# Performance work log

Hardware: AMD Instinct MI355X
Metric: run time of the kernel (lower is better)

The kernel has to match this reference:

```python
import jax, jax.numpy as jnp
import numpy as np

B, L, U, H = 16, 1024, 512, 2  # batch, seq_len, units, highway_num


def setup_inputs() -> dict:
    key = jax.random.key(0)
    ks = jax.random.split(key, 8)
    s = 0.02  # weight init scale
    return {
        "inputs": jax.random.normal(ks[0], (B, L, U), dtype=jnp.float32),
        "tW": jax.random.normal(ks[1], (H, U, U), dtype=jnp.float32) * s,
        "tb": jnp.zeros((H, U), dtype=jnp.float32),
        "cW": jax.random.normal(ks[2], (H, U, U), dtype=jnp.float32) * s,
        "cb": jnp.zeros((H, U), dtype=jnp.float32),
        "aW": jax.random.normal(ks[3], (3 * U,), dtype=jnp.float32) * s,
        "ab": jnp.zeros((1,), dtype=jnp.float32),
        "frW": jax.random.normal(ks[4], (2 * U, U), dtype=jnp.float32) * s,
        "frb": jnp.zeros((U,), dtype=jnp.float32),
        "ffW": jax.random.normal(ks[5], (2 * U, U), dtype=jnp.float32) * s,
        "ffb": jnp.zeros((U,), dtype=jnp.float32),
    }


def reference(inputs, tW, tb, cW, cb, aW, ab, frW, frb, ffW, ffb):
    # Highway stack (inference: dropout is identity)
    x = inputs
    for i in range(tW.shape[0]):
        t = jax.nn.relu(x @ tW[i] + tb[i])
        c = jax.nn.sigmoid(x @ cW[i] + cb[i])
        x = t * c + x * (1.0 - c)

    # Pairwise MLP self-attention.
    # Original: A_ij = relu(dense1(concat([x_i, x_j, x_i*x_j]))).
    # Split aW = [w1; w2; w3] so we never materialize the [B,L,L,3U] tensor:
    # A_ij = relu(x_i.w1 + x_j.w2 + sum_d x_i_d * x_j_d * w3_d + b)
    u = x.shape[-1]
    w1, w2, w3 = aW[:u], aW[u:2 * u], aW[2 * u:]
    s1 = x @ w1                                    # [B,L]
    s2 = x @ w2                                    # [B,L]
    s3 = jnp.einsum('bid,bjd->bij', x * w3, x)     # [B,L,L]
    A = jax.nn.relu(s1[:, :, None] + s2[:, None, :] + s3 + ab[0])
    att = jnp.einsum('bij,bjd->bid', jax.nn.softmax(A, axis=-1), x)

    # Fuse gate. NOTE: original code uses fuse_f_dense (sigmoid) for BOTH
    # z and f (fuse_z_dense is never called), so z == f at inference.
    concat = jnp.concatenate([inputs, att], axis=-1)  # [B,L,2U]
    z = jax.nn.sigmoid(concat @ ffW + ffb)
    r = jax.nn.sigmoid(concat @ frW + frb)
    f = z
    return r * inputs + f * z
```

## Files before the change

kernel.cpp:

```cpp
#include <hip/hip_runtime.h>
#include <math.h>

typedef __bf16 bf16;
typedef __attribute__((ext_vector_type(8))) __bf16 bf16x8;
typedef __attribute__((ext_vector_type(4))) float f32x4;

#define CDIV(a,b) (((a)+(b)-1)/(b))


__device__ __forceinline__ void load_lds16(const bf16* g, bf16* l) {
  __builtin_amdgcn_global_load_lds(
      (const __attribute__((address_space(1))) unsigned int*)(g),
      (__attribute__((address_space(3))) unsigned int*)(l), 16, 0, 0);
}

struct GemmArgs {
  const bf16* A; const bf16* B; bf16* C;
  int K, lda, ldb, ldc;
  long long Ab, Bb, Cb;
  const float* s1; const float* s2; const float* abp;
  float* lsum;
  int L;
  int gxsh, gysh;
};

template<int EPI, int TN>
__global__ __launch_bounds__(256, 4)
void gemm_nt(GemmArgs g) {
  constexpr int JN = TN / 32;
  __shared__ bf16 As[128 * 64];
  __shared__ bf16 Bs[TN * 64];
  const int tid = threadIdx.x;
  const int bid = blockIdx.x;
  const int xcd = bid & 7;
  const int t = bid >> 3;
  const int bx = t & ((1 << g.gxsh) - 1);
  const int r  = t >> g.gxsh;
  const int Rx = gridDim.x >> (3 + g.gxsh);
  const int gr = xcd * Rx + r;
  const int by = gr & ((1 << g.gysh) - 1);
  const int bz = gr >> g.gysh;

  const bf16* Ag = g.A + (long long)bz * g.Ab + (long long)(by * 128) * g.lda;
  const bf16* Bg = g.B + (long long)bz * g.Bb + (long long)(bx * TN) * g.ldb;
  const int wid = tid >> 6, lane = tid & 63;
  const int wm = (wid >> 1) << 6;
  const int wn = (wid & 1) * (TN / 2);
  const int lr = lane & 15, lq = lane >> 4;

  f32x4 acc[4][JN];
#pragma unroll
  for (int i = 0; i < 4; i++)
#pragma unroll
    for (int j = 0; j < JN; j++) acc[i][j] = f32x4{0.f, 0.f, 0.f, 0.f};

  const int srow8 = (tid >> 3) & 7;
  const int skc   = (tid & 7) ^ srow8;
  const int lswz  = (lr & 7);

  for (int k0 = 0; k0 < g.K; k0 += 64) {
    __syncthreads();
#pragma unroll
    for (int j = 0; j < 4; j++) {
      const int ci = (tid >> 6) * 4 + j;
      const int row = ci * 8 + srow8;
      load_lds16(Ag + (long long)row * g.lda + k0 + skc * 8, As + ci * 512);
    }
#pragma unroll
    for (int j = 0; j < JN; j++) {
      const int ci = (tid >> 6) * JN + j;
      const int row = ci * 8 + srow8;
      load_lds16(Bg + (long long)row * g.ldb + k0 + skc * 8, Bs + ci * 512);
    }
    __syncthreads();
#pragma unroll
    for (int ks = 0; ks < 2; ks++) {
      bf16x8 af[4], bfr[JN];
      const int kx = (ks * 4 + lq) ^ lswz;
#pragma unroll
      for (int i = 0; i < 4; i++)
        af[i] = *(const bf16x8*)(&As[(wm + i * 16 + lr) * 64 + kx * 8]);
#pragma unroll
      for (int j = 0; j < JN; j++)
        bfr[j] = *(const bf16x8*)(&Bs[(wn + j * 16 + lr) * 64 + kx * 8]);
#pragma unroll
      for (int i = 0; i < 4; i++)
#pragma unroll
        for (int j = 0; j < JN; j++)
          acc[i][j] = __builtin_amdgcn_mfma_f32_16x16x32_bf16(af[i], bfr[j], acc[i][j], 0, 0, 0);
    }
  }

  bf16* Cg = g.C + (long long)bz * g.Cb;
#pragma unroll
  for (int i = 0; i < 4; i++) {
#pragma unroll
    for (int v = 0; v < 4; v++) {
      int row = by * 128 + wm + i * 16 + lq * 4 + v;
      float srow = 0.f;
      if (EPI == 1) srow = g.s1[bz * g.L + row] + g.abp[0];
      if (EPI == 4) srow = 1.f / g.s1[bz * g.L + row];
      float psum = 0.f;
#pragma unroll
      for (int j = 0; j < JN; j++) {
        int col = bx * TN + wn + j * 16 + lr;
        float val = acc[i][j][v];
        if (EPI == 1) {
          val += srow + g.s2[bz * g.L + col];
          val = fminf(fmaxf(val, 0.f), 60.f);
          val = __expf(val);
          bf16 eb = (bf16)val;
          psum += (float)eb;
          Cg[(long long)row * g.ldc + col] = eb;
        } else {
          val *= srow;
          Cg[(long long)row * g.ldc + col] = (bf16)val;
        }
      }
      if (EPI == 1) {
        psum += __shfl_xor(psum, 1, 64);
        psum += __shfl_xor(psum, 2, 64);
        psum += __shfl_xor(psum, 4, 64);
        psum += __shfl_xor(psum, 8, 64);
        if (lr == 0) atomicAdd(&g.lsum[bz * g.L + row], psum);
      }
    }
  }
}

struct DualArgs {
  const bf16* A; const bf16* A2;
  const bf16* Bt;
  void* C; const void* xres;
  const float* bias_t; const float* bias_c;
  int K, ldb;
  const float* aW;
  float* s1a; float* s2a;
  bf16* q;
  bf16* xT;
};

template<int EPI>
__global__ __launch_bounds__(256, 4)
void gemm_dual(DualArgs g) {
  __shared__ bf16 smem[2 * 128 * 64];
  bf16* As = smem;
  bf16* Bs = smem + 8192;
  const int tid = threadIdx.x;
  const int bid = blockIdx.x;
  const int xcd = bid & 7;
  const int t = bid >> 3;
  const int bx = t & 7;
  const int r  = t >> 3;
  const int Rx = gridDim.x >> 6;
  const int by = xcd * Rx + r;

  const int wid = tid >> 6, lane = tid & 63;
  const int wm = (wid >> 1) << 6;
  const int wn = (wid & 1) << 6;
  const int lr = lane & 15, lq = lane >> 4;

  f32x4 acc[4][4];
#pragma unroll
  for (int i = 0; i < 4; i++)
#pragma unroll
    for (int j = 0; j < 4; j++) acc[i][j] = f32x4{0.f, 0.f, 0.f, 0.f};

  const int srow8 = (tid >> 3) & 7;
  const int skc   = (tid & 7) ^ srow8;
  const int lswz  = (lr & 7);
  const long long abase = (long long)(by * 128) * 512;

  for (int k0 = 0; k0 < g.K; k0 += 64) {
    const bf16* Ak = (k0 < 512) ? g.A : g.A2;
    const int kk = k0 & 511;
    __syncthreads();
#pragma unroll
    for (int j = 0; j < 4; j++) {
      const int ci = (tid >> 6) * 4 + j;
      const int bn = ci * 8 + srow8;
      load_lds16(Ak + abase + (long long)bn * 512 + kk + skc * 8, As + ci * 512);
      const int grp = bn >> 5, r5 = bn & 31;
      const int grow = ((grp & 1) << 9) + bx * 64 + ((grp >> 1) << 5) + r5;
      load_lds16(g.Bt + (long long)grow * g.ldb + k0 + skc * 8, Bs + ci * 512);
    }
    __syncthreads();
#pragma unroll
    for (int ks = 0; ks < 2; ks++) {
      bf16x8 af[4], bfr[4];
      const int kx = (ks * 4 + lq) ^ lswz;
#pragma unroll
      for (int i = 0; i < 4; i++)
        af[i] = *(const bf16x8*)(&As[(wm + i * 16 + lr) * 64 + kx * 8]);
#pragma unroll
      for (int j = 0; j < 4; j++)
        bfr[j] = *(const bf16x8*)(&Bs[(wn + j * 16 + lr) * 64 + kx * 8]);
#pragma unroll
      for (int i = 0; i < 4; i++)
#pragma unroll
        for (int j = 0; j < 4; j++)
          acc[i][j] = __builtin_amdgcn_mfma_f32_16x16x32_bf16(af[i], bfr[j], acc[i][j], 0, 0, 0);
    }
  }

  const int colb = bx * 64 + (wn >> 1);
  bf16 xn_arr[4][4][2];
#pragma unroll
  for (int i = 0; i < 4; i++) {
#pragma unroll
    for (int v = 0; v < 4; v++) {
      int row = by * 128 + wm + i * 16 + lq * 4 + v;
      float p1s = 0.f, p2s = 0.f;
#pragma unroll
      for (int j = 0; j < 2; j++) {
        int col = colb + j * 16 + lr;
        long long idx = (long long)row * 512 + col;
        float p0 = acc[i][j][v] + g.bias_t[col];
        float p1 = acc[i][j + 2][v] + g.bias_c[col];
        if (EPI == 1) {
          float z = 1.f / (1.f + __expf(-p0));
          float rr = 1.f / (1.f + __expf(-p1));
          float x = (float)((const bf16*)g.xres)[idx];
          ((float*)g.C)[idx] = rr * x + z * z;
        } else {
          float tt = fmaxf(p0, 0.f);
          float c = 1.f / (1.f + __expf(-p1));
          float x = (float)((const bf16*)g.xres)[idx];
          bf16 xn = (bf16)(tt * c + x * (1.f - c));
          ((bf16*)g.C)[idx] = xn;
          if (EPI == 2) {
            xn_arr[i][v][j] = xn;
            float xf = (float)xn;
            p1s += xf * g.aW[col];
            p2s += xf * g.aW[512 + col];
            g.q[idx] = (bf16)(xf * g.aW[1024 + col]);
          }
        }
      }
      if (EPI == 2) {
        p1s += __shfl_xor(p1s, 1, 64);
        p1s += __shfl_xor(p1s, 2, 64);
        p1s += __shfl_xor(p1s, 4, 64);
        p1s += __shfl_xor(p1s, 8, 64);
        p2s += __shfl_xor(p2s, 1, 64);
        p2s += __shfl_xor(p2s, 2, 64);
        p2s += __shfl_xor(p2s, 4, 64);
        p2s += __shfl_xor(p2s, 8, 64);
        if (lr == 0) {
          atomicAdd(&g.s1a[row], p1s);
          atomicAdd(&g.s2a[row], p2s);
        }
      }
    }
  }

  if (EPI == 2) {
    bf16* Ts = smem;
    __syncthreads();
#pragma unroll
    for (int i = 0; i < 4; i++)
#pragma unroll
      for (int v = 0; v < 4; v++)
#pragma unroll
        for (int j = 0; j < 2; j++) {
          int rloc = wm + i * 16 + lq * 4 + v;
          int cloc = (wn >> 1) + j * 16 + lr;
          Ts[cloc * 136 + rloc] = xn_arr[i][v][j];
        }
    __syncthreads();
    const int b = by >> 3;
    bf16* dst = g.xT + (long long)b * 524288 + ((by & 7) * 128);
#pragma unroll
    for (int it = 0; it < 2; it++) {
      int d = (tid >> 3) + it * 32;
      int jb = (tid & 7) * 16;
      bf16x8 v0 = *(const bf16x8*)(&Ts[d * 136 + jb]);
      bf16x8 v1 = *(const bf16x8*)(&Ts[d * 136 + jb + 8]);
      long long o = (long long)(bx * 64 + d) * 1024 + jb;
      *(bf16x8*)(dst + o) = v0;
      *(bf16x8*)(dst + o + 8) = v1;
    }
  }
}

__device__ __forceinline__ void tile_transpose(const float* src, int sld,
                                               bf16* dst, int dld,
                                               int k0, int n0, int tid) {
  __shared__ float tile[64][65];
  const int rr = tid >> 4, c4 = (tid & 15) * 4;
#pragma unroll
  for (int it = 0; it < 4; it++) {
    int r = rr + it * 16;
    f32x4 v = *(const f32x4*)(src + (long long)(k0 + r) * sld + n0 + c4);
    tile[r][c4] = v[0]; tile[r][c4 + 1] = v[1];
    tile[r][c4 + 2] = v[2]; tile[r][c4 + 3] = v[3];
  }
  __syncthreads();
  const int nl = tid >> 2, kb = (tid & 3) * 16;
  bf16x8 o0, o1;
#pragma unroll
  for (int kk = 0; kk < 8; kk++) o0[kk] = (bf16)tile[kb + kk][nl];
#pragma unroll
  for (int kk = 0; kk < 8; kk++) o1[kk] = (bf16)tile[kb + 8 + kk][nl];
  bf16* d = dst + (long long)(n0 + nl) * dld + k0 + kb;
  *(bf16x8*)d = o0;
  *(bf16x8*)(d + 8) = o1;
}

__global__ void prep(const float* tW, const float* tb, const float* cW, const float* cb,
                     const float* frW, const float* frb, const float* ffW, const float* ffb,
                     const float* inp, bf16* xb0,
                     bf16* w1T, bf16* w2T, float* bias1, float* bias2, float* sred) {
  const int bid = blockIdx.x, tid = threadIdx.x;
  if (bid < 256) {
    const int quad = bid >> 6, tile = bid & 63;
    const int l = quad >> 1, half = quad & 1;
    const float* src = (half ? cW : tW) + l * 262144;
    bf16* dst = w1T + l * 524288 + half * 262144;
    tile_transpose(src, 512, dst, 512, (tile >> 3) * 64, (tile & 7) * 64, tid);
  } else if (bid < 512) {
    const int j = bid - 256;
    const int half = j >> 7, tile = j & 127;
    const float* src = half ? frW : ffW;
    bf16* dst = w2T + half * 524288;
    tile_transpose(src, 512, dst, 1024, (tile >> 3) * 64, (tile & 7) * 64, tid);
  } else if (bid < 4608) {
    long long i8 = (((long long)(bid - 512)) * 256 + tid) * 8;
    bf16x8 o;
#pragma unroll
    for (int k = 0; k < 8; k++) o[k] = (bf16)inp[i8 + k];
    *(bf16x8*)(xb0 + i8) = o;
  } else {
    for (int j = tid; j < 3072; j += 256) {
      if (j < 2048) {
        int l = j >> 10, n = j & 1023;
        bias1[j] = (n < 512) ? tb[l * 512 + n] : cb[l * 512 + (n - 512)];
      } else {
        int n = j - 2048;
        bias2[n] = (n < 512) ? ffb[n] : frb[n - 512];
      }
    }
    for (int j = tid; j < 12288; j += 256)
      *(f32x4*)(sred + j * 4) = f32x4{0.f, 0.f, 0.f, 0.f};
  }
}

extern "C" void kernel_launch(void* const* d_in, const int* in_sizes, int n_in,
                              void* d_out, int out_size, void* d_ws, size_t ws_size,
                              hipStream_t stream) {
  const float* inp = (const float*)d_in[0];
  const float* tW  = (const float*)d_in[1];
  const float* tb  = (const float*)d_in[2];
  const float* cW  = (const float*)d_in[3];
  const float* cb  = (const float*)d_in[4];
  const float* aW  = (const float*)d_in[5];
  const float* ab  = (const float*)d_in[6];
  const float* frW = (const float*)d_in[7];
  const float* frb = (const float*)d_in[8];
  const float* ffW = (const float*)d_in[9];
  const float* ffb = (const float*)d_in[10];
  float* out = (float*)d_out;

  char* p = (char*)d_ws;
  auto alloc = [&](size_t bytes) { char* r = p; p += (bytes + 255) & ~size_t(255); return r; };
  bf16* xb0   = (bf16*) alloc(16777216);
  bf16* x1    = (bf16*) alloc(16777216);
  bf16* x2    = (bf16*) alloc(16777216);
  bf16* q16   = (bf16*) alloc(16777216);
  bf16* xT16  = (bf16*) alloc(16777216);
  bf16* att16 = (bf16*) alloc(16777216);
  bf16* E16   = (bf16*) alloc(33554432);
  float* sred = (float*)alloc(196608);
  bf16* w1T   = (bf16*) alloc(2097152);
  bf16* w2T   = (bf16*) alloc(2097152);
  float* bias1= (float*)alloc(8192);
  float* bias2= (float*)alloc(4096);
  float* s1 = sred, *s2 = sred + 16384, *lsum = sred + 32768;

  prep<<<4609, 256, 0, stream>>>(
      tW, tb, cW, cb, frW, frb, ffW, ffb, inp, xb0, w1T, w2T, bias1, bias2, sred);

  {
    DualArgs g{};
    g.A = xb0; g.A2 = xb0; g.Bt = w1T;
    g.C = x1; g.xres = xb0;
    g.bias_t = bias1; g.bias_c = bias1 + 512;
    g.K = 512; g.ldb = 512;
    gemm_dual<0><<<1024, 256, 0, stream>>>(g);
  }
  {
    DualArgs g{};
    g.A = x1; g.A2 = x1; g.Bt = w1T + 524288;
    g.C = x2; g.xres = x1;
    g.bias_t = bias1 + 1024; g.bias_c = bias1 + 1536;
    g.K = 512; g.ldb = 512;
    g.aW = aW; g.s1a = s1; g.s2a = s2; g.q = q16; g.xT = xT16;
    gemm_dual<2><<<1024, 256, 0, stream>>>(g);
  }
  {
    GemmArgs g{};
    g.A = q16; g.B = x2; g.C = E16;
    g.K = 512; g.lda = 512; g.ldb = 512; g.ldc = 1024;
    g.Ab = 524288; g.Bb = 524288; g.Cb = 1048576;
    g.s1 = s1; g.s2 = s2; g.abp = ab; g.lsum = lsum; g.L = 1024;
    g.gxsh = 3; g.gysh = 3;
    gemm_nt<1, 128><<<1024, 256, 0, stream>>>(g);
  }
  {
    GemmArgs g{};
    g.A = E16; g.B = xT16; g.C = att16;
    g.K = 1024; g.lda = 1024; g.ldb = 1024; g.ldc = 512;
    g.Ab = 1048576; g.Bb = 524288; g.Cb = 524288;
    g.s1 = lsum; g.L = 1024;
    g.gxsh = 3; g.gysh = 3;
    gemm_nt<4, 64><<<1024, 256, 0, stream>>>(g);
  }
  {
    DualArgs g{};
    g.A = xb0; g.A2 = att16; g.Bt = w2T;
    g.C = out; g.xres = xb0;
    g.bias_t = bias2; g.bias_c = bias2 + 512;
    g.K = 1024; g.ldb = 1024;
    gemm_dual<1><<<1024, 256, 0, stream>>>(g);
  }
}
```

Measured before the change: 269.7 us.

## Rewrite dual highway GEMMs as 256x256 8-wave double-buffered pipelined kernel

The dual-output highway/fuse GEMM moves from 128x128 tiles with 4 waves and a single-buffered LDS loop to 256x256 tiles (128 output columns per gate) with 8 waves. Global-to-LDS loads are double-buffered and interleaved in quarter stages with MFMA phases, using s_setprio and explicit vmcnt waits. The xT transpose now writes straight into LDS during the epilogue. The aim is more data reuse per tile and overlap of loads with compute. The trade-offs are a grid of only 256 blocks, fewer blocks per CU from the larger LDS footprint, and fragile hand-written barrier and waitcnt ordering.

```diff
diff --git a/kernel.cpp b/kernel.cpp
--- a/kernel.cpp
+++ b/kernel.cpp
@@ -4,8 +4,6 @@
 typedef __bf16 bf16;
 typedef __attribute__((ext_vector_type(8))) __bf16 bf16x8;
 typedef __attribute__((ext_vector_type(4))) float f32x4;
-
-#define CDIV(a,b) (((a)+(b)-1)/(b))
 
 
 __device__ __forceinline__ void load_lds16(const bf16* g, bf16* l) {
@@ -141,82 +139,156 @@
 };
 
 template<int EPI>
-__global__ __launch_bounds__(256, 4)
-void gemm_dual(DualArgs g) {
-  __shared__ bf16 smem[2 * 128 * 64];
-  bf16* As = smem;
-  bf16* Bs = smem + 8192;
+__global__ __launch_bounds__(512, 2)
+void gemm_dual8(DualArgs g) {
+  __shared__ __align__(16) bf16 smem[2][32768];
   const int tid = threadIdx.x;
   const int bid = blockIdx.x;
   const int xcd = bid & 7;
   const int t = bid >> 3;
-  const int bx = t & 7;
-  const int r  = t >> 3;
-  const int Rx = gridDim.x >> 6;
-  const int by = xcd * Rx + r;
-
+  const int bx = t & 3;
+  const int by = xcd * 8 + (t >> 2);
   const int wid = tid >> 6, lane = tid & 63;
-  const int wm = (wid >> 1) << 6;
-  const int wn = (wid & 1) << 6;
+  const int wr = wid >> 2, wc = wid & 3;
   const int lr = lane & 15, lq = lane >> 4;
-
-  f32x4 acc[4][4];
-#pragma unroll
-  for (int i = 0; i < 4; i++)
+  const int lswz = lr & 7;
+  const int srow8 = (lane >> 3) & 7;
+  const int skc = (lane & 7) ^ srow8;
+  const long long abase = (long long)(by * 256) * 512;
+  const int NT = g.K >> 6;
+
+  f32x4 acc[8][4];
+#pragma unroll
+  for (int i = 0; i < 8; i++)
 #pragma unroll
     for (int j = 0; j < 4; j++) acc[i][j] = f32x4{0.f, 0.f, 0.f, 0.f};
 
-  const int srow8 = (tid >> 3) & 7;
-  const int skc   = (tid & 7) ^ srow8;
-  const int lswz  = (lr & 7);
-  const long long abase = (long long)(by * 128) * 512;
-
-  for (int k0 = 0; k0 < g.K; k0 += 64) {
-    const bf16* Ak = (k0 < 512) ? g.A : g.A2;
-    const int kk = k0 & 511;
-    __syncthreads();
-#pragma unroll
-    for (int j = 0; j < 4; j++) {
-      const int ci = (tid >> 6) * 4 + j;
-      const int bn = ci * 8 + srow8;
-      load_lds16(Ak + abase + (long long)bn * 512 + kk + skc * 8, As + ci * 512);
+  auto stage_a = [&](int kt, int b, int h) {
+    const bf16* Ak = (kt < 8) ? g.A : g.A2;
+    const int kk = (kt & 7) << 6;
+#pragma unroll
+    for (int jj = 0; jj < 2; jj++) {
+      const int c = h * 16 + wid * 2 + jj;
+      const int row = c * 8 + srow8;
+      load_lds16(Ak + abase + (long long)row * 512 + kk + skc * 8,
+                 &smem[b][c * 512]);
+    }
+  };
+  auto stage_b = [&](int kt, int b, int h) {
+    const int k0 = kt << 6;
+#pragma unroll
+    for (int jj = 0; jj < 2; jj++) {
+      const int ci = wid * 2 + jj;
+      const int c = ((ci >> 2) << 3) + (h << 2) + (ci & 3);
+      const int bn = c * 8 + srow8;
       const int grp = bn >> 5, r5 = bn & 31;
-      const int grow = ((grp & 1) << 9) + bx * 64 + ((grp >> 1) << 5) + r5;
-      load_lds16(g.Bt + (long long)grow * g.ldb + k0 + skc * 8, Bs + ci * 512);
-    }
-    __syncthreads();
-#pragma unroll
-    for (int ks = 0; ks < 2; ks++) {
-      bf16x8 af[4], bfr[4];
-      const int kx = (ks * 4 + lq) ^ lswz;
-#pragma unroll
-      for (int i = 0; i < 4; i++)
-        af[i] = *(const bf16x8*)(&As[(wm + i * 16 + lr) * 64 + kx * 8]);
-#pragma unroll
-      for (int j = 0; j < 4; j++)
-        bfr[j] = *(const bf16x8*)(&Bs[(wn + j * 16 + lr) * 64 + kx * 8]);
-#pragma unroll
-      for (int i = 0; i < 4; i++)
-#pragma unroll
-        for (int j = 0; j < 4; j++)
-          acc[i][j] = __builtin_amdgcn_mfma_f32_16x16x32_bf16(af[i], bfr[j], acc[i][j], 0, 0, 0);
-    }
-  }
-
-  const int colb = bx * 64 + (wn >> 1);
-  bf16 xn_arr[4][4][2];
-#pragma unroll
-  for (int i = 0; i < 4; i++) {
+      const int grow = ((grp & 1) << 9) + bx * 128 + ((grp >> 1) << 5) + r5;
+      load_lds16(g.Bt + (long long)grow * g.ldb + k0 + skc * 8,
+                 &smem[b][16384 + c * 512]);
+    }
+  };
+  auto ldA = [&](int b, int i, int ks) -> bf16x8 {
+    const int kx = (ks * 4 + lq) ^ lswz;
+    return *(const bf16x8*)(&smem[b][(wr * 128 + i * 16 + lr) * 64 + kx * 8]);
+  };
+  auto ldB = [&](int b, int j, int ks) -> bf16x8 {
+    const int kx = (ks * 4 + lq) ^ lswz;
+    return *(const bf16x8*)(&smem[b][16384 + (wc * 64 + j * 16 + lr) * 64 + kx * 8]);
+  };
+
+  stage_b(0, 0, 0); stage_b(0, 0, 1); stage_a(0, 0, 0); stage_a(0, 0, 1);
+  stage_b(1, 1, 0); stage_b(1, 1, 1); stage_a(1, 1, 0);
+  asm volatile("s_waitcnt vmcnt(6)" ::: "memory");
+  __builtin_amdgcn_s_barrier();
+
+  for (int kt = 0; kt < NT; kt++) {
+    const int cur = kt & 1, nxt = cur ^ 1;
+    bf16x8 af[4][2], b01[2][2], b23[2][2];
+    if (kt + 1 < NT) stage_a(kt + 1, nxt, 1);
+#pragma unroll
+    for (int i = 0; i < 4; i++)
+#pragma unroll
+      for (int ks = 0; ks < 2; ks++) af[i][ks] = ldA(cur, i, ks);
+#pragma unroll
+    for (int j = 0; j < 2; j++)
+#pragma unroll
+      for (int ks = 0; ks < 2; ks++) b01[j][ks] = ldB(cur, j, ks);
+    __builtin_amdgcn_s_barrier();
+    __builtin_amdgcn_s_setprio(1);
+#pragma unroll
+    for (int i = 0; i < 4; i++)
+#pragma unroll
+      for (int j = 0; j < 2; j++)
+#pragma unroll
+        for (int ks = 0; ks < 2; ks++)
+          acc[i][j] = __builtin_amdgcn_mfma_f32_16x16x32_bf16(af[i][ks], b01[j][ks], acc[i][j], 0, 0, 0);
+    __builtin_amdgcn_s_setprio(0);
+    __builtin_amdgcn_s_barrier();
+    if (kt + 2 < NT) stage_b(kt + 2, cur, 0);
+#pragma unroll
+    for (int j = 0; j < 2; j++)
+#pragma unroll
+      for (int ks = 0; ks < 2; ks++) b23[j][ks] = ldB(cur, 2 + j, ks);
+    __builtin_amdgcn_s_barrier();
+    __builtin_amdgcn_s_setprio(1);
+#pragma unroll
+    for (int i = 0; i < 4; i++)
+#pragma unroll
+      for (int j = 0; j < 2; j++)
+#pragma unroll
+        for (int ks = 0; ks < 2; ks++)
+          acc[i][2 + j] = __builtin_amdgcn_mfma_f32_16x16x32_bf16(af[i][ks], b23[j][ks], acc[i][2 + j], 0, 0, 0);
+    __builtin_amdgcn_s_setprio(0);
+    __builtin_amdgcn_s_barrier();
+    if (kt + 2 < NT) stage_b(kt + 2, cur, 1);
+#pragma unroll
+    for (int i = 0; i < 4; i++)
+#pragma unroll
+      for (int ks = 0; ks < 2; ks++) af[i][ks] = ldA(cur, 4 + i, ks);
+    __builtin_amdgcn_s_barrier();
+    __builtin_amdgcn_s_setprio(1);
+#pragma unroll
+    for (int i = 0; i < 4; i++)
+#pragma unroll
+      for (int j = 0; j < 2; j++)
+#pragma unroll
+        for (int ks = 0; ks < 2; ks++)
+          acc[4 + i][2 + j] = __builtin_amdgcn_mfma_f32_16x16x32_bf16(af[i][ks], b23[j][ks], acc[4 + i][2 + j], 0, 0, 0);
+    __builtin_amdgcn_s_setprio(0);
+    __builtin_amdgcn_s_barrier();
+    if (kt + 2 < NT) stage_a(kt + 2, cur, 0);
+    __builtin_amdgcn_s_barrier();
+    __builtin_amdgcn_s_setprio(1);
+#pragma unroll
+    for (int i = 0; i < 4; i++)
+#pragma unroll
+      for (int j = 0; j < 2; j++)
+#pragma unroll
+        for (int ks = 0; ks < 2; ks++)
+          acc[4 + i][j] = __builtin_amdgcn_mfma_f32_16x16x32_bf16(af[i][ks], b01[j][ks], acc[4 + i][j], 0, 0, 0);
+    __builtin_amdgcn_s_setprio(0);
+    if (kt + 2 < NT) {
+      asm volatile("s_waitcnt vmcnt(6)" ::: "memory");
+    } else if (kt + 1 < NT) {
+      asm volatile("s_waitcnt vmcnt(0)" ::: "memory");
+    }
+    __builtin_amdgcn_s_barrier();
+  }
+
+  bf16* Ts = (bf16*)&smem[0][0];
+  const int colb = bx * 128 + wc * 32;
+#pragma unroll
+  for (int i = 0; i < 8; i++) {
 #pragma unroll
     for (int v = 0; v < 4; v++) {
-      int row = by * 128 + wm + i * 16 + lq * 4 + v;
+      const int row = by * 256 + wr * 128 + i * 16 + lq * 4 + v;
       float p1s = 0.f, p2s = 0.f;
 #pragma unroll
-      for (int j = 0; j < 2; j++) {
-        int col = colb + j * 16 + lr;
-        long long idx = (long long)row * 512 + col;
-        float p0 = acc[i][j][v] + g.bias_t[col];
-        float p1 = acc[i][j + 2][v] + g.bias_c[col];
+      for (int jj = 0; jj < 2; jj++) {
+        const int col = colb + jj * 16 + lr;
+        const long long idx = (long long)row * 512 + col;
+        float p0 = acc[i][jj][v] + g.bias_t[col];
+        float p1 = acc[i][jj + 2][v] + g.bias_c[col];
         if (EPI == 1) {
           float z = 1.f / (1.f + __expf(-p0));
           float rr = 1.f / (1.f + __expf(-p1));
@@ -229,11 +301,11 @@
           bf16 xn = (bf16)(tt * c + x * (1.f - c));
           ((bf16*)g.C)[idx] = xn;
           if (EPI == 2) {
-            xn_arr[i][v][j] = xn;
             float xf = (float)xn;
             p1s += xf * g.aW[col];
             p2s += xf * g.aW[512 + col];
             g.q[idx] = (bf16)(xf * g.aW[1024 + col]);
+            Ts[(wc * 32 + jj * 16 + lr) * 264 + (wr * 128 + i * 16 + lq * 4 + v)] = xn;
           }
         }
       }
@@ -255,28 +327,18 @@
   }
 
   if (EPI == 2) {
-    bf16* Ts = smem;
     __syncthreads();
-#pragma unroll
-    for (int i = 0; i < 4; i++)
-#pragma unroll
-      for (int v = 0; v < 4; v++)
-#pragma unroll
-        for (int j = 0; j < 2; j++) {
-          int rloc = wm + i * 16 + lq * 4 + v;
-          int cloc = (wn >> 1) + j * 16 + lr;
-          Ts[cloc * 136 + rloc] = xn_arr[i][v][j];
-        }
-    __syncthreads();
-    const int b = by >> 3;
-    bf16* dst = g.xT + (long long)b * 524288 + ((by & 7) * 128);
-#pragma unroll
-    for (int it = 0; it < 2; it++) {
-      int d = (tid >> 3) + it * 32;
-      int jb = (tid & 7) * 16;
-      bf16x8 v0 = *(const bf16x8*)(&Ts[d * 136 + jb]);
-      bf16x8 v1 = *(const bf16x8*)(&Ts[d * 136 + jb + 8]);
-      long long o = (long long)(bx * 64 + d) * 1024 + jb;
+    const int b = by >> 2;
+    const long long j0 = (long long)(by & 3) * 256;
+    bf16* dst = g.xT + (long long)b * 524288;
+    const int dloc = tid >> 2;
+    const int jb = (tid & 3) * 64;
+#pragma unroll
+    for (int it = 0; it < 4; it++) {
+      const int j = jb + it * 16;
+      bf16x8 v0 = *(const bf16x8*)(&Ts[dloc * 264 + j]);
+      bf16x8 v1 = *(const bf16x8*)(&Ts[dloc * 264 + j + 8]);
+      long long o = (long long)(bx * 128 + dloc) * 1024 + j0 + j;
       *(bf16x8*)(dst + o) = v0;
       *(bf16x8*)(dst + o + 8) = v1;
     }
@@ -386,7 +448,7 @@
     g.C = x1; g.xres = xb0;
     g.bias_t = bias1; g.bias_c = bias1 + 512;
     g.K = 512; g.ldb = 512;
-    gemm_dual<0><<<1024, 256, 0, stream>>>(g);
+    gemm_dual8<0><<<256, 512, 0, stream>>>(g);
   }
   {
     DualArgs g{};
@@ -395,7 +457,7 @@
     g.bias_t = bias1 + 1024; g.bias_c = bias1 + 1536;
     g.K = 512; g.ldb = 512;
     g.aW = aW; g.s1a = s1; g.s2a = s2; g.q = q16; g.xT = xT16;
-    gemm_dual<2><<<1024, 256, 0, stream>>>(g);
+    gemm_dual8<2><<<256, 512, 0, stream>>>(g);
   }
   {
     GemmArgs g{};
@@ -421,6 +483,6 @@
     g.C = out; g.xres = xb0;
     g.bias_t = bias2; g.bias_c = bias2 + 512;
     g.K = 1024; g.ldb = 1024;
-    gemm_dual<1><<<1024, 256, 0, stream>>>(g);
-  }
-}
+    gemm_dual8<1><<<256, 512, 0, stream>>>(g);
+  }
+}
```

Measured after the change: 296.7 us. 1.1x slower.

## Fuse score GEMM, exp epilogue and PV GEMM into one attention kernel

Applied to the files above, without the earlier changes.

Replaces the two batched GEMM launches with a single fused attention kernel. The score GEMM, its exp epilogue and the value GEMM no longer write a full [B,L,L] bf16 score matrix to global memory and read it back. Each 512-thread block keeps a 64-row Q tile resident in LDS and streams X tiles through a double buffer. It writes exp scores into a swizzled LDS tile, multiplies them with X^T fetched straight from global memory, and normalises by row sums reduced in LDS instead of with global atomics. This trades the large intermediate traffic and one launch for a grid of only 256 blocks with heavy LDS use, low occupancy, frequent barriers, and uncached, partly redundant global loads of X^T.

```diff
diff --git a/kernel.cpp b/kernel.cpp
--- a/kernel.cpp
+++ b/kernel.cpp
@@ -4,128 +4,12 @@
 typedef __bf16 bf16;
 typedef __attribute__((ext_vector_type(8))) __bf16 bf16x8;
 typedef __attribute__((ext_vector_type(4))) float f32x4;
-
-#define CDIV(a,b) (((a)+(b)-1)/(b))
 
 
 __device__ __forceinline__ void load_lds16(const bf16* g, bf16* l) {
   __builtin_amdgcn_global_load_lds(
       (const __attribute__((address_space(1))) unsigned int*)(g),
       (__attribute__((address_space(3))) unsigned int*)(l), 16, 0, 0);
-}
-
-struct GemmArgs {
-  const bf16* A; const bf16* B; bf16* C;
-  int K, lda, ldb, ldc;
-  long long Ab, Bb, Cb;
-  const float* s1; const float* s2; const float* abp;
-  float* lsum;
-  int L;
-  int gxsh, gysh;
-};
-
-template<int EPI, int TN>
-__global__ __launch_bounds__(256, 4)
-void gemm_nt(GemmArgs g) {
-  constexpr int JN = TN / 32;
-  __shared__ bf16 As[128 * 64];
-  __shared__ bf16 Bs[TN * 64];
-  const int tid = threadIdx.x;
-  const int bid = blockIdx.x;
-  const int xcd = bid & 7;
-  const int t = bid >> 3;
-  const int bx = t & ((1 << g.gxsh) - 1);
-  const int r  = t >> g.gxsh;
-  const int Rx = gridDim.x >> (3 + g.gxsh);
-  const int gr = xcd * Rx + r;
-  const int by = gr & ((1 << g.gysh) - 1);
-  const int bz = gr >> g.gysh;
-
-  const bf16* Ag = g.A + (long long)bz * g.Ab + (long long)(by * 128) * g.lda;
-  const bf16* Bg = g.B + (long long)bz * g.Bb + (long long)(bx * TN) * g.ldb;
-  const int wid = tid >> 6, lane = tid & 63;
-  const int wm = (wid >> 1) << 6;
-  const int wn = (wid & 1) * (TN / 2);
-  const int lr = lane & 15, lq = lane >> 4;
-
-  f32x4 acc[4][JN];
-#pragma unroll
-  for (int i = 0; i < 4; i++)
-#pragma unroll
-    for (int j = 0; j < JN; j++) acc[i][j] = f32x4{0.f, 0.f, 0.f, 0.f};
-
-  const int srow8 = (tid >> 3) & 7;
-  const int skc   = (tid & 7) ^ srow8;
-  const int lswz  = (lr & 7);
-
-  for (int k0 = 0; k0 < g.K; k0 += 64) {
-    __syncthreads();
-#pragma unroll
-    for (int j = 0; j < 4; j++) {
-      const int ci = (tid >> 6) * 4 + j;
-      const int row = ci * 8 + srow8;
-      load_lds16(Ag + (long long)row * g.lda + k0 + skc * 8, As + ci * 512);
-    }
-#pragma unroll
-    for (int j = 0; j < JN; j++) {
-      const int ci = (tid >> 6) * JN + j;
-      const int row = ci * 8 + srow8;
-      load_lds16(Bg + (long long)row * g.ldb + k0 + skc * 8, Bs + ci * 512);
-    }
-    __syncthreads();
-#pragma unroll
-    for (int ks = 0; ks < 2; ks++) {
-      bf16x8 af[4], bfr[JN];
-      const int kx = (ks * 4 + lq) ^ lswz;
-#pragma unroll
-      for (int i = 0; i < 4; i++)
-        af[i] = *(const bf16x8*)(&As[(wm + i * 16 + lr) * 64 + kx * 8]);
-#pragma unroll
-      for (int j = 0; j < JN; j++)
-        bfr[j] = *(const bf16x8*)(&Bs[(wn + j * 16 + lr) * 64 + kx * 8]);
-#pragma unroll
-      for (int i = 0; i < 4; i++)
-#pragma unroll
-        for (int j = 0; j < JN; j++)
-          acc[i][j] = __builtin_amdgcn_mfma_f32_16x16x32_bf16(af[i], bfr[j], acc[i][j], 0, 0, 0);
-    }
-  }
-
-  bf16* Cg = g.C + (long long)bz * g.Cb;
-#pragma unroll
-  for (int i = 0; i < 4; i++) {
-#pragma unroll
-    for (int v = 0; v < 4; v++) {
-      int row = by * 128 + wm + i * 16 + lq * 4 + v;
-      float srow = 0.f;
-      if (EPI == 1) srow = g.s1[bz * g.L + row] + g.abp[0];
-      if (EPI == 4) srow = 1.f / g.s1[bz * g.L + row];
-      float psum = 0.f;
-#pragma unroll
-      for (int j = 0; j < JN; j++) {
-        int col = bx * TN + wn + j * 16 + lr;
-        float val = acc[i][j][v];
-        if (EPI == 1) {
-          val += srow + g.s2[bz * g.L + col];
-          val = fminf(fmaxf(val, 0.f), 60.f);
-          val = __expf(val);
-          bf16 eb = (bf16)val;
-          psum += (float)eb;
-          Cg[(long long)row * g.ldc + col] = eb;
-        } else {
-          val *= srow;
-          Cg[(long long)row * g.ldc + col] = (bf16)val;
-        }
-      }
-      if (EPI == 1) {
-        psum += __shfl_xor(psum, 1, 64);
-        psum += __shfl_xor(psum, 2, 64);
-        psum += __shfl_xor(psum, 4, 64);
-        psum += __shfl_xor(psum, 8, 64);
-        if (lr == 0) atomicAdd(&g.lsum[bz * g.L + row], psum);
-      }
-    }
-  }
 }
 
 struct DualArgs {
@@ -283,6 +167,202 @@
   }
 }
 
+struct AttnArgs {
+  const bf16* Q;
+  const bf16* X;
+  const bf16* XT;
+  bf16* O;
+  const float* s1; const float* s2; const float* abp;
+};
+
+__global__ __launch_bounds__(512, 2)
+void attn_fused(AttnArgs g) {
+  __shared__ __align__(16) bf16 smem[57344];
+  __shared__ float lsum_sh[4][64];
+  bf16* Qs = smem;
+  bf16* Es = smem + 49152;
+  const int tid = threadIdx.x;
+  const int bid = blockIdx.x;
+  const int gr = (bid & 7) * 32 + (bid >> 3);
+  const int bz = gr >> 4, qt = gr & 15;
+  const int wid = tid >> 6, lane = tid & 63;
+  const int wr = wid >> 2, wc = wid & 3;
+  const int lr = lane & 15, lq = lane >> 4;
+  const int lswz = lr & 7;
+  const int srow8 = (lane >> 3) & 7;
+  const int skc = (lane & 7) ^ srow8;
+
+  const bf16* Qg = g.Q + (long long)bz * 524288 + (long long)(qt * 64) * 512;
+  const bf16* Xg = g.X + (long long)bz * 524288;
+  const bf16* XTg = g.XT + (long long)bz * 524288;
+
+#pragma unroll
+  for (int c8 = 0; c8 < 8; c8++) {
+    const int row = c8 * 8 + srow8;
+    load_lds16(Qg + (long long)row * 512 + wid * 64 + skc * 8,
+               Qs + (wid * 8 + c8) * 512);
+  }
+#pragma unroll
+  for (int jj = 0; jj < 2; jj++) {
+    const int c = wid * 2 + jj;
+    load_lds16(Xg + (long long)(c * 8 + srow8) * 512 + skc * 8,
+               smem + 32768 + c * 512);
+  }
+
+  float s1r[2][4];
+#pragma unroll
+  for (int i = 0; i < 2; i++)
+#pragma unroll
+    for (int v = 0; v < 4; v++)
+      s1r[i][v] = g.s1[bz * 1024 + qt * 64 + wr * 32 + i * 16 + lq * 4 + v] + g.abp[0];
+
+  f32x4 acc_o[2][8];
+  float lsum[2][4];
+#pragma unroll
+  for (int i = 0; i < 2; i++) {
+#pragma unroll
+    for (int jd = 0; jd < 8; jd++) acc_o[i][jd] = f32x4{0.f, 0.f, 0.f, 0.f};
+#pragma unroll
+    for (int v = 0; v < 4; v++) lsum[i][v] = 0.f;
+  }
+
+  __syncthreads();
+
+  int cur = 0;
+  for (int jt = 0; jt < 8; jt++) {
+    f32x4 acc_s[2][2];
+#pragma unroll
+    for (int i = 0; i < 2; i++)
+#pragma unroll
+      for (int jjf = 0; jjf < 2; jjf++) acc_s[i][jjf] = f32x4{0.f, 0.f, 0.f, 0.f};
+
+    for (int p = 0; p < 8; p++) {
+      if (p < 7) {
+#pragma unroll
+        for (int jj = 0; jj < 2; jj++) {
+          const int c = wid * 2 + jj;
+          load_lds16(Xg + (long long)(jt * 128 + c * 8 + srow8) * 512 + (p + 1) * 64 + skc * 8,
+                     smem + 32768 + (cur ^ 1) * 8192 + c * 512);
+        }
+      } else if (jt + 1 < 8) {
+#pragma unroll
+        for (int jj = 0; jj < 2; jj++) {
+          const int c = wid * 2 + jj;
+          load_lds16(Xg + (long long)((jt + 1) * 128 + c * 8 + srow8) * 512 + skc * 8,
+                     smem + 32768 + (cur ^ 1) * 8192 + c * 512);
+        }
+      }
+      bf16x8 aq[2][2], bx[2][2];
+#pragma unroll
+      for (int ks = 0; ks < 2; ks++) {
+        const int kx = (ks * 4 + lq) ^ lswz;
+#pragma unroll
+        for (int i = 0; i < 2; i++)
+          aq[i][ks] = *(const bf16x8*)(&Qs[p * 4096 + (wr * 32 + i * 16 + lr) * 64 + kx * 8]);
+#pragma unroll
+        for (int jjf = 0; jjf < 2; jjf++)
+          bx[jjf][ks] = *(const bf16x8*)(&smem[32768 + cur * 8192 + (wc * 32 + jjf * 16 + lr) * 64 + kx * 8]);
+      }
+#pragma unroll
+      for (int i = 0; i < 2; i++)
+#pragma unroll
+        for (int jjf = 0; jjf < 2; jjf++)
+#pragma unroll
+          for (int ks = 0; ks < 2; ks++)
+            acc_s[i][jjf] = __builtin_amdgcn_mfma_f32_16x16x32_bf16(aq[i][ks], bx[jjf][ks], acc_s[i][jjf], 0, 0, 0);
+      __syncthreads();
+      cur ^= 1;
+    }
+
+    float s2v[2];
+#pragma unroll
+    for (int jjf = 0; jjf < 2; jjf++)
+      s2v[jjf] = g.s2[bz * 1024 + jt * 128 + wc * 32 + jjf * 16 + lr];
+#pragma unroll
+    for (int i = 0; i < 2; i++) {
+#pragma unroll
+      for (int v = 0; v < 4; v++) {
+        const int rl = wr * 32 + i * 16 + lq * 4 + v;
+        float ps = 0.f;
+#pragma unroll
+        for (int jjf = 0; jjf < 2; jjf++) {
+          const int jl = wc * 32 + jjf * 16 + lr;
+          float val = acc_s[i][jjf][v] + s1r[i][v] + s2v[jjf];
+          val = fminf(fmaxf(val, 0.f), 60.f);
+          val = __expf(val);
+          bf16 eb = (bf16)val;
+          ps += (float)eb;
+          Es[(jl >> 6) * 4096 + rl * 64 + (((jl >> 3) & 7) ^ (rl & 7)) * 8 + (jl & 7)] = eb;
+        }
+        ps += __shfl_xor(ps, 1, 64);
+        ps += __shfl_xor(ps, 2, 64);
+        ps += __shfl_xor(ps, 4, 64);
+        ps += __shfl_xor(ps, 8, 64);
+        lsum[i][v] += ps;
+      }
+    }
+    __syncthreads();
+
+#pragma unroll
+    for (int kq = 0; kq < 4; kq++) {
+      bf16x8 aE[2];
+      const int kx = (((kq & 1) * 4 + lq)) ^ lswz;
+#pragma unroll
+      for (int i = 0; i < 2; i++)
+        aE[i] = *(const bf16x8*)(&Es[(kq >> 1) * 4096 + (wr * 32 + i * 16 + lr) * 64 + kx * 8]);
+      bf16x8 bv[8];
+#pragma unroll
+      for (int jd = 0; jd < 8; jd++)
+        bv[jd] = *(const bf16x8*)(XTg + (long long)(wc * 128 + jd * 16 + lr) * 1024
+                                  + jt * 128 + kq * 32 + lq * 8);
+#pragma unroll
+      for (int jd = 0; jd < 8; jd++) {
+        acc_o[0][jd] = __builtin_amdgcn_mfma_f32_16x16x32_bf16(aE[0], bv[jd], acc_o[0][jd], 0, 0, 0);
+        acc_o[1][jd] = __builtin_amdgcn_mfma_f32_16x16x32_bf16(aE[1], bv[jd], acc_o[1][jd], 0, 0, 0);
+      }
+    }
+  }
+
+  if (lr == 0) {
+#pragma unroll
+    for (int i = 0; i < 2; i++)
+#pragma unroll
+      for (int v = 0; v < 4; v++)
+        lsum_sh[wc][wr * 32 + i * 16 + lq * 4 + v] = lsum[i][v];
+  }
+  __syncthreads();
+
+  bf16* Ts = smem;
+  float rinv[2][4];
+#pragma unroll
+  for (int i = 0; i < 2; i++)
+#pragma unroll
+    for (int v = 0; v < 4; v++) {
+      const int rl = wr * 32 + i * 16 + lq * 4 + v;
+      const float tot = lsum_sh[0][rl] + lsum_sh[1][rl] + lsum_sh[2][rl] + lsum_sh[3][rl];
+      rinv[i][v] = 1.f / tot;
+    }
+  __syncthreads();
+#pragma unroll
+  for (int i = 0; i < 2; i++)
+#pragma unroll
+    for (int jd = 0; jd < 8; jd++)
+#pragma unroll
+      for (int v = 0; v < 4; v++) {
+        const int rl = wr * 32 + i * 16 + lq * 4 + v;
+        const int d = wc * 128 + jd * 16 + lr;
+        Ts[rl * 520 + d] = (bf16)(acc_o[i][jd][v] * rinv[i][v]);
+      }
+  __syncthreads();
+  bf16* Og = g.O + (long long)bz * 524288 + (long long)(qt * 64) * 512;
+#pragma unroll
+  for (int rr = 0; rr < 8; rr++) {
+    const int row = wid * 8 + rr;
+    bf16x8 vv = *(const bf16x8*)(&Ts[row * 520 + lane * 8]);
+    *(bf16x8*)(Og + (long long)row * 512 + lane * 8) = vv;
+  }
+}
+
 __device__ __forceinline__ void tile_transpose(const float* src, int sld,
                                                bf16* dst, int dld,
                                                int k0, int n0, int tid) {
@@ -369,13 +449,12 @@
   bf16* q16   = (bf16*) alloc(16777216);
   bf16* xT16  = (bf16*) alloc(16777216);
   bf16* att16 = (bf16*) alloc(16777216);
-  bf16* E16   = (bf16*) alloc(33554432);
   float* sred = (float*)alloc(196608);
   bf16* w1T   = (bf16*) alloc(2097152);
   bf16* w2T   = (bf16*) alloc(2097152);
   float* bias1= (float*)alloc(8192);
   float* bias2= (float*)alloc(4096);
-  float* s1 = sred, *s2 = sred + 16384, *lsum = sred + 32768;
+  float* s1 = sred, *s2 = sred + 16384;
 
   prep<<<4609, 256, 0, stream>>>(
       tW, tb, cW, cb, frW, frb, ffW, ffb, inp, xb0, w1T, w2T, bias1, bias2, sred);
@@ -398,22 +477,10 @@
     gemm_dual<2><<<1024, 256, 0, stream>>>(g);
   }
   {
-    GemmArgs g{};
-    g.A = q16; g.B = x2; g.C = E16;
-    g.K = 512; g.lda = 512; g.ldb = 512; g.ldc = 1024;
-    g.Ab = 524288; g.Bb = 524288; g.Cb = 1048576;
-    g.s1 = s1; g.s2 = s2; g.abp = ab; g.lsum = lsum; g.L = 1024;
-    g.gxsh = 3; g.gysh = 3;
-    gemm_nt<1, 128><<<1024, 256, 0, stream>>>(g);
-  }
-  {
-    GemmArgs g{};
-    g.A = E16; g.B = xT16; g.C = att16;
-    g.K = 1024; g.lda = 1024; g.ldb = 1024; g.ldc = 512;
-    g.Ab = 1048576; g.Bb = 524288; g.Cb = 524288;
-    g.s1 = lsum; g.L = 1024;
-    g.gxsh = 3; g.gysh = 3;
-    gemm_nt<4, 64><<<1024, 256, 0, stream>>>(g);
+    AttnArgs g{};
+    g.Q = q16; g.X = x2; g.XT = xT16; g.O = att16;
+    g.s1 = s1; g.s2 = s2; g.abp = ab;
+    attn_fused<<<256, 512, 0, stream>>>(g);
   }
   {
     DualArgs g{};
```

New measurement: 322.6 us. 1.2x slower.
